# Performance work log

Hardware: AMD Instinct MI355X
Metric: run time of the kernel (lower is better)

The kernel has to match this reference:

```python
import jax, jax.numpy as jnp
import numpy as np

M, N = 4096, 4096


def _makhoul_perm(n):
    # Makhoul even/odd reordering: v[k] = x[2k] for k < ceil(n/2),
    # v[n-1-k] = x[2k+1] for the rest. This is the same input permutation
    # the dct2_fft2 kernel applies before its rfft2.
    idx = np.empty(n, dtype=np.int32)
    half = (n + 1) // 2
    idx[:half] = 2 * np.arange(half)
    idx[half:] = 2 * (n - 1 - np.arange(half, n)) + 1
    return jnp.asarray(idx)


def _dct2_1d_last(x):
    # Unnormalized DCT-II along the last axis via a same-length FFT plus
    # twiddle (expk) multiply:  C[k] = Re( exp(-i*pi*k/(2n)) * FFT(v)[k] )
    # which equals sum_m x[m] * cos(pi*k*(2m+1)/(2n)).
    n = x.shape[-1]
    v = jnp.take(x, _makhoul_perm(n), axis=-1)
    V = jnp.fft.fft(v, axis=-1)
    k = jnp.arange(n)
    expk = jnp.exp((-1j * np.pi / (2.0 * n)) * k)  # twiddle factors (expkM/expkN)
    return jnp.real(V * expk).astype(x.dtype)


def setup_inputs() -> dict:
    key = jax.random.key(0)
    x = jax.random.normal(key, (M, N), dtype=jnp.float32)
    return {"x": x}


def reference(x):
    # Separable 2D DCT-II: along axis -1 (uses expkN), then axis -2 (expkM).
    y = _dct2_1d_last(x)        # DCT over columns index (length N)
    y = _dct2_1d_last(y.T).T    # DCT over rows index (length M)
    return y
```

## Files before the change

kernel.cpp:

```cpp
#include <hip/hip_runtime.h>
#include <stdint.h>


#define NF 4096

__device__ __forceinline__ int physi(int e) { return e ^ ((e >> 4) & 15); }

__device__ __forceinline__ float2 cadd(float2 a, float2 b) {
    float2 r; r.x = a.x + b.x; r.y = a.y + b.y; return r;
}
__device__ __forceinline__ float2 csub(float2 a, float2 b) {
    float2 r; r.x = a.x - b.x; r.y = a.y - b.y; return r;
}
__device__ __forceinline__ float2 cmulc(float2 a, float2 b) {
    float2 r; r.x = a.x * b.x - a.y * b.y; r.y = a.x * b.y + a.y * b.x; return r;
}
__device__ __forceinline__ float2 rotm(float2 a) {
    float2 r; r.x = a.y; r.y = -a.x; return r;
}

__global__ __launch_bounds__(256) void setup_tables(float* __restrict__ tw,
                                                    float* __restrict__ ek) {
    int idx = blockIdx.x * 256 + threadIdx.x;
    if (idx < 4416) {
        int p, u; float denom;
        if (idx < 64)       { p = idx >> 3;         u = idx & 7;  denom = 64.0f; }
        else if (idx < 320) { int r = idx - 64;  p = r >> 4; u = r & 15; denom = 256.0f; }
        else                { int r = idx - 320; p = r >> 4; u = r & 15; denom = 4096.0f; }
        float phi = (float)(p * u) * (6.283185307179586f / denom);
        float s, c; __sincosf(phi, &s, &c);
        tw[2 * idx]     = c;
        tw[2 * idx + 1] = -s;
    } else if (idx < 8512) {
        int k = idx - 4416;
        float th = (float)k * (3.141592653589793f / 8192.0f);
        float s, c; __sincosf(th, &s, &c);
        ek[2 * k]     = c;
        ek[2 * k + 1] = s;
    }
}

#define RADIX8(Xv, E0, E1, E2, E3, O0, g1, g2, g3)                             \
    float2 t0 = cadd(Xv[0], Xv[4]), t1 = csub(Xv[0], Xv[4]);                   \
    float2 t2 = cadd(Xv[2], Xv[6]), t3 = csub(Xv[2], Xv[6]);                   \
    float2 E0 = cadd(t0, t2), E2 = csub(t0, t2);                               \
    float2 r3 = rotm(t3);                                                      \
    float2 E1 = cadd(t1, r3), E3 = csub(t1, r3);                               \
    float2 s0 = cadd(Xv[1], Xv[5]), s1 = csub(Xv[1], Xv[5]);                   \
    float2 s2 = cadd(Xv[3], Xv[7]), s3 = csub(Xv[3], Xv[7]);                   \
    float2 O0 = cadd(s0, s2), O2 = csub(s0, s2);                               \
    float2 r7 = rotm(s3);                                                      \
    float2 O1 = cadd(s1, r7), O3 = csub(s1, r7);                               \
    const float SQ = 0.7071067811865476f;                                      \
    float2 g1; g1.x = SQ * (O1.x + O1.y); g1.y = SQ * (O1.y - O1.x);           \
    float2 g2 = rotm(O2);                                                      \
    float2 g3; g3.x = SQ * (O3.y - O3.x); g3.y = -SQ * (O3.x + O3.y);

#define RADIX8_OUT(Xv, Ov)                                                     \
    {                                                                          \
        RADIX8(Xv, E0, E1, E2, E3, O0, g1, g2, g3)                             \
        Ov[0] = cadd(E0, O0); Ov[1] = cadd(E1, g1);                            \
        Ov[2] = cadd(E2, g2); Ov[3] = cadd(E3, g3);                            \
        Ov[4] = csub(E0, O0); Ov[5] = csub(E1, g1);                            \
        Ov[6] = csub(E2, g2); Ov[7] = csub(E3, g3);                            \
    }

__device__ __forceinline__ void dft16(float2* x) {
    float2 E[8], O[8];
    {
        float2 a[8];
        #pragma unroll
        for (int m = 0; m < 8; ++m) a[m] = x[2 * m];
        RADIX8_OUT(a, E)
    }
    {
        float2 a[8];
        #pragma unroll
        for (int m = 0; m < 8; ++m) a[m] = x[2 * m + 1];
        RADIX8_OUT(a, O)
    }
    const float2 W1 = { 0.9238795325112867f, -0.3826834323650898f};
    const float2 W2 = { 0.7071067811865476f, -0.7071067811865476f};
    const float2 W3 = { 0.3826834323650898f, -0.9238795325112867f};
    const float2 W5 = {-0.3826834323650898f, -0.9238795325112867f};
    const float2 W6 = {-0.7071067811865476f, -0.7071067811865476f};
    const float2 W7 = {-0.9238795325112867f, -0.3826834323650898f};
    float2 t;
    x[0] = cadd(E[0], O[0]);  x[8]  = csub(E[0], O[0]);
    t = cmulc(O[1], W1); x[1] = cadd(E[1], t); x[9]  = csub(E[1], t);
    t = cmulc(O[2], W2); x[2] = cadd(E[2], t); x[10] = csub(E[2], t);
    t = cmulc(O[3], W3); x[3] = cadd(E[3], t); x[11] = csub(E[3], t);
    t = rotm(O[4]);      x[4] = cadd(E[4], t); x[12] = csub(E[4], t);
    t = cmulc(O[5], W5); x[5] = cadd(E[5], t); x[13] = csub(E[5], t);
    t = cmulc(O[6], W6); x[6] = cadd(E[6], t); x[14] = csub(E[6], t);
    t = cmulc(O[7], W7); x[7] = cadd(E[7], t); x[15] = csub(E[7], t);
}

__global__ __launch_bounds__(256) void dct_rows(const float* __restrict__ In,
                                                float* __restrict__ Out,
                                                const float* __restrict__ tw,
                                                const float* __restrict__ ek) {
    __shared__ float2 buf[NF];
    const int j = threadIdx.x;
    const int b = blockIdx.x;
    const float* in0 = In + (size_t)(2 * b) * NF;
    const float* in1 = in0 + NF;
    float* out0 = Out + (size_t)b * NF;
    float* out1 = Out + (size_t)(4095 - b) * NF;

    const float4* i40 = (const float4*)in0;
    const float4* i41 = (const float4*)in1;
    #pragma unroll
    for (int c = 0; c < 4; ++c) {
        float4 a0 = i40[j + 256 * c];
        float4 a1 = i41[j + 256 * c];
        int nb = 2 * j + 512 * c;
        float2 z0; z0.x = a0.x; z0.y = a1.x;
        float2 z1; z1.x = a0.z; z1.y = a1.z;
        float2 z2; z2.x = a0.y; z2.y = a1.y;
        float2 z3; z3.x = a0.w; z3.y = a1.w;
        buf[physi(nb)]        = z0;
        buf[physi(nb + 1)]    = z1;
        buf[physi(4095 - nb)] = z2;
        buf[physi(4094 - nb)] = z3;
    }
    __syncthreads();

    float2 x[16];

    #pragma unroll
    for (int k = 0; k < 16; ++k)
        x[k] = buf[physi(j + 256 * k)];
    dft16(x);
    __syncthreads();
    #pragma unroll
    for (int i = 0; i < 16; ++i)
        buf[physi(16 * j + i)] = x[i];
    __syncthreads();

    {
        const int p = j & 15, q = j >> 4;
        #pragma unroll
        for (int k = 0; k < 16; ++k)
            x[k] = buf[physi(j + 256 * k)];
        const float2* twp = (const float2*)tw + 64 + p * 16;
        #pragma unroll
        for (int k = 1; k < 16; ++k)
            x[k] = cmulc(x[k], twp[k]);
        dft16(x);
        __syncthreads();
        int wb = p + 256 * q;
        #pragma unroll
        for (int i = 0; i < 16; ++i)
            buf[physi(wb + 16 * i)] = x[i];
        __syncthreads();
    }

    {
        #pragma unroll
        for (int k = 0; k < 16; ++k)
            x[k] = buf[physi(j + 256 * k)];
        const float2* twp = (const float2*)tw + 320 + j * 16;
        #pragma unroll
        for (int k = 1; k < 16; ++k)
            x[k] = cmulc(x[k], twp[k]);
        dft16(x);
        #pragma unroll
        for (int i = 0; i < 16; ++i)
            buf[physi(j + 256 * i)] = x[i];
    }
    __syncthreads();

    #pragma unroll
    for (int i = 0; i < 16; ++i) {
        int k = j + 256 * i;
        int m = (NF - k) & (NF - 1);
        float2 Zk = x[i];
        float2 Zm = buf[physi(m)];
        float2 E = ((const float2*)ek)[k];
        out0[k] = 0.5f * ((Zk.x + Zm.x) * E.x + (Zk.y - Zm.y) * E.y);
        out1[k] = 0.5f * ((Zk.y + Zm.y) * E.x - (Zk.x - Zm.x) * E.y);
    }
}

__global__ __launch_bounds__(256) void col_fft1(const float* __restrict__ V,
                                                float* __restrict__ S,
                                                const float* __restrict__ tw) {
    __shared__ float2 T[64][64];
    __shared__ float2 w64[64];
    const int ct = blockIdx.x, n1 = blockIdx.y;
    const int t = threadIdx.x;
    const int cp4 = t & 31, j = t >> 5;
    const float4* in4 = (const float4*)V + (size_t)ct * 32 + cp4;

    if (t < 64) {
        int m = (n1 * t) & 4095;
        float phi = (float)m * -1.5339807878856412e-3f;
        float s, c; __sincosf(phi, &s, &c);
        float2 w; w.x = c; w.y = s;
        w64[t] = w;
    }

    float2 xA[8], xB[8];
    #pragma unroll
    for (int k = 0; k < 8; ++k) {
        float4 v4 = in4[(size_t)(n1 + 64 * (j + 8 * k)) * 1024];
        xA[k].x = v4.x; xA[k].y = v4.y;
        xB[k].x = v4.z; xB[k].y = v4.w;
    }
    {
        float2 rA[8], rB[8];
        RADIX8_OUT(xA, rA)
        RADIX8_OUT(xB, rB)
        #pragma unroll
        for (int i = 0; i < 8; ++i) {
            float4 w; w.x = rA[i].x; w.y = rA[i].y; w.z = rB[i].x; w.w = rB[i].y;
            *(float4*)&T[8 * j + i][2 * cp4] = w;
        }
    }
    __syncthreads();

    float2 oA[8], oB[8];
    {
        #pragma unroll
        for (int k = 0; k < 8; ++k) {
            float4 v4 = *(const float4*)&T[j + 8 * k][2 * cp4];
            xA[k].x = v4.x; xA[k].y = v4.y;
            xB[k].x = v4.z; xB[k].y = v4.w;
        }
        const float2* twp = (const float2*)tw + j * 8;
        #pragma unroll
        for (int k = 1; k < 8; ++k) {
            xA[k] = cmulc(xA[k], twp[k]);
            xB[k] = cmulc(xB[k], twp[k]);
        }
        RADIX8_OUT(xA, oA)
        RADIX8_OUT(xB, oB)
    }

    float4* out4 = (float4*)S + (size_t)ct * 32 + cp4;
    #pragma unroll
    for (int i = 0; i < 8; ++i) {
        int k2 = j + 8 * i;
        float2 hA = cmulc(oA[i], w64[k2]);
        float2 hB = cmulc(oB[i], w64[k2]);
        float4 w; w.x = hA.x; w.y = hA.y; w.z = hB.x; w.w = hB.y;
        out4[(size_t)(64 * k2 + n1) * 1024] = w;
    }
}

__global__ __launch_bounds__(512) void col_fft2(const float* __restrict__ S,
                                                float* __restrict__ Out,
                                                const float* __restrict__ tw,
                                                const float* __restrict__ ek) {
    __shared__ float2 T[2][64][32];
    const int ct = blockIdx.x, bp = blockIdx.y;
    const int ga = bp, gb = (bp == 0) ? 32 : 64 - bp;
    const int t = threadIdx.x;
    const int cp = t & 31, j = (t >> 5) & 7, gi = t >> 8;
    const int g = gi ? gb : ga;
    const float2* inb = (const float2*)S + (size_t)ct * 32 + cp;

    float2 x[8];
    #pragma unroll
    for (int k = 0; k < 8; ++k)
        x[k] = inb[(size_t)(64 * g + j + 8 * k) * 2048];
    {
        float2 r[8];
        RADIX8_OUT(x, r)
        #pragma unroll
        for (int i = 0; i < 8; ++i)
            T[gi][8 * j + i][cp] = r[i];
    }
    __syncthreads();

    float2 o[8];
    {
        #pragma unroll
        for (int k = 0; k < 8; ++k)
            x[k] = T[gi][j + 8 * k][cp];
        const float2* twp = (const float2*)tw + j * 8;
        #pragma unroll
        for (int k = 1; k < 8; ++k)
            x[k] = cmulc(x[k], twp[k]);
        RADIX8_OUT(x, o)
        #pragma unroll
        for (int i = 0; i < 8; ++i)
            T[gi][j + 8 * i][cp] = o[i];
    }
    __syncthreads();

    float2* outb = (float2*)Out + (size_t)ct * 32 + cp;
    #pragma unroll
    for (int i = 0; i < 8; ++i) {
        int k = 64 * (j + 8 * i) + g;
        int m = (NF - k) & (NF - 1);
        int gp = m & 63, k1p = m >> 6;
        float2 Zk = o[i];
        float2 Zm = T[(gp == ga) ? 0 : 1][k1p][cp];
        float2 E = ((const float2*)ek)[k];
        float2 r;
        r.x = 0.5f * ((Zk.x + Zm.x) * E.x + (Zk.y - Zm.y) * E.y);
        r.y = 0.5f * ((Zk.y + Zm.y) * E.x - (Zk.x - Zm.x) * E.y);
        outb[(size_t)k * 2048] = r;
    }
}

extern "C" void kernel_launch(void* const* d_in, const int* in_sizes, int n_in,
                              void* d_out, int out_size, void* d_ws, size_t ws_size,
                              hipStream_t stream) {
    const float* x = (const float*)d_in[0];
    float* out = (float*)d_out;

    float* tw = (float*)d_ws;
    float* ek = tw + 8832;
    float* B1 = ek + 8192;
    if (ws_size < (size_t)68096 + (size_t)NF * NF * sizeof(float)) return;

    setup_tables<<<34, 256, 0, stream>>>(tw, ek);
    dct_rows<<<NF / 2, 256, 0, stream>>>(x, out, tw, ek);
    col_fft1<<<dim3(32, 64), 256, 0, stream>>>(out, B1, tw);
    col_fft2<<<dim3(64, 32), 512, 0, stream>>>(B1, out, tw, ek);
}
```

Baseline: 167.6 us.

## Process four tiles per block with register prefetch of the next tile's global loads

All three FFT kernels now loop over four tiles per block, and the grids shrink by four. The next tile's global data is loaded into registers while the current tile is written to shared memory, so load latency overlaps with the FFT work. __syncthreads is replaced by a custom barrier that waits only on LDS counters, leaving the outstanding global prefetch loads in flight across the barrier. The cost is fewer blocks (512 or fewer per kernel) and higher register pressure, which may lower occupancy and parallelism on a 256-CU device.

```diff
diff --git a/kernel.cpp b/kernel.cpp
--- a/kernel.cpp
+++ b/kernel.cpp
@@ -3,6 +3,13 @@
 
 
 #define NF 4096
+
+#define LBAR()                                                                 \
+    do {                                                                       \
+        asm volatile("s_waitcnt lgkmcnt(0)" ::: "memory");                     \
+        __builtin_amdgcn_s_barrier();                                          \
+        __builtin_amdgcn_sched_barrier(0);                                     \
+    } while (0)
 
 __device__ __forceinline__ int physi(int e) { return e ^ ((e >> 4) & 15); }
 
@@ -102,84 +109,97 @@
                                                 const float* __restrict__ ek) {
     __shared__ float2 buf[NF];
     const int j = threadIdx.x;
-    const int b = blockIdx.x;
-    const float* in0 = In + (size_t)(2 * b) * NF;
-    const float* in1 = in0 + NF;
-    float* out0 = Out + (size_t)b * NF;
-    float* out1 = Out + (size_t)(4095 - b) * NF;
-
-    const float4* i40 = (const float4*)in0;
-    const float4* i41 = (const float4*)in1;
-    #pragma unroll
-    for (int c = 0; c < 4; ++c) {
-        float4 a0 = i40[j + 256 * c];
-        float4 a1 = i41[j + 256 * c];
-        int nb = 2 * j + 512 * c;
-        float2 z0; z0.x = a0.x; z0.y = a1.x;
-        float2 z1; z1.x = a0.z; z1.y = a1.z;
-        float2 z2; z2.x = a0.y; z2.y = a1.y;
-        float2 z3; z3.x = a0.w; z3.y = a1.w;
-        buf[physi(nb)]        = z0;
-        buf[physi(nb + 1)]    = z1;
-        buf[physi(4095 - nb)] = z2;
-        buf[physi(4094 - nb)] = z3;
-    }
-    __syncthreads();
-
-    float2 x[16];
-
-    #pragma unroll
-    for (int k = 0; k < 16; ++k)
-        x[k] = buf[physi(j + 256 * k)];
-    dft16(x);
-    __syncthreads();
-    #pragma unroll
-    for (int i = 0; i < 16; ++i)
-        buf[physi(16 * j + i)] = x[i];
-    __syncthreads();
-
-    {
-        const int p = j & 15, q = j >> 4;
+    const int b0 = blockIdx.x * 4;
+
+    float4 ca[4], cb[4];
+    {
+        const float4* i40 = (const float4*)(In + (size_t)(2 * b0) * NF);
+        const float4* i41 = i40 + 1024;
+        #pragma unroll
+        for (int c = 0; c < 4; ++c) { ca[c] = i40[j + 256 * c]; cb[c] = i41[j + 256 * c]; }
+    }
+
+    for (int tt = 0; tt < 4; ++tt) {
+        const int b = b0 + tt;
+        float* out0 = Out + (size_t)b * NF;
+        float* out1 = Out + (size_t)(4095 - b) * NF;
+
+        #pragma unroll
+        for (int c = 0; c < 4; ++c) {
+            int nb = 2 * j + 512 * c;
+            float2 z0; z0.x = ca[c].x; z0.y = cb[c].x;
+            float2 z1; z1.x = ca[c].z; z1.y = cb[c].z;
+            float2 z2; z2.x = ca[c].y; z2.y = cb[c].y;
+            float2 z3; z3.x = ca[c].w; z3.y = cb[c].w;
+            buf[physi(nb)]        = z0;
+            buf[physi(nb + 1)]    = z1;
+            buf[physi(4095 - nb)] = z2;
+            buf[physi(4094 - nb)] = z3;
+        }
+        if (tt < 3) {
+            const float4* n40 = (const float4*)(In + (size_t)(2 * (b + 1)) * NF);
+            const float4* n41 = n40 + 1024;
+            #pragma unroll
+            for (int c = 0; c < 4; ++c) { ca[c] = n40[j + 256 * c]; cb[c] = n41[j + 256 * c]; }
+        }
+        LBAR();
+
+        float2 x[16];
+
         #pragma unroll
         for (int k = 0; k < 16; ++k)
             x[k] = buf[physi(j + 256 * k)];
-        const float2* twp = (const float2*)tw + 64 + p * 16;
-        #pragma unroll
-        for (int k = 1; k < 16; ++k)
-            x[k] = cmulc(x[k], twp[k]);
         dft16(x);
-        __syncthreads();
-        int wb = p + 256 * q;
+        LBAR();
         #pragma unroll
         for (int i = 0; i < 16; ++i)
-            buf[physi(wb + 16 * i)] = x[i];
-        __syncthreads();
-    }
-
-    {
-        #pragma unroll
-        for (int k = 0; k < 16; ++k)
-            x[k] = buf[physi(j + 256 * k)];
-        const float2* twp = (const float2*)tw + 320 + j * 16;
-        #pragma unroll
-        for (int k = 1; k < 16; ++k)
-            x[k] = cmulc(x[k], twp[k]);
-        dft16(x);
-        #pragma unroll
-        for (int i = 0; i < 16; ++i)
-            buf[physi(j + 256 * i)] = x[i];
-    }
-    __syncthreads();
-
-    #pragma unroll
-    for (int i = 0; i < 16; ++i) {
-        int k = j + 256 * i;
-        int m = (NF - k) & (NF - 1);
-        float2 Zk = x[i];
-        float2 Zm = buf[physi(m)];
-        float2 E = ((const float2*)ek)[k];
-        out0[k] = 0.5f * ((Zk.x + Zm.x) * E.x + (Zk.y - Zm.y) * E.y);
-        out1[k] = 0.5f * ((Zk.y + Zm.y) * E.x - (Zk.x - Zm.x) * E.y);
+            buf[physi(16 * j + i)] = x[i];
+        LBAR();
+
+        {
+            const int p = j & 15, q = j >> 4;
+            #pragma unroll
+            for (int k = 0; k < 16; ++k)
+                x[k] = buf[physi(j + 256 * k)];
+            const float2* twp = (const float2*)tw + 64 + p * 16;
+            #pragma unroll
+            for (int k = 1; k < 16; ++k)
+                x[k] = cmulc(x[k], twp[k]);
+            dft16(x);
+            LBAR();
+            int wb = p + 256 * q;
+            #pragma unroll
+            for (int i = 0; i < 16; ++i)
+                buf[physi(wb + 16 * i)] = x[i];
+            LBAR();
+        }
+
+        {
+            #pragma unroll
+            for (int k = 0; k < 16; ++k)
+                x[k] = buf[physi(j + 256 * k)];
+            const float2* twp = (const float2*)tw + 320 + j * 16;
+            #pragma unroll
+            for (int k = 1; k < 16; ++k)
+                x[k] = cmulc(x[k], twp[k]);
+            dft16(x);
+            #pragma unroll
+            for (int i = 0; i < 16; ++i)
+                buf[physi(j + 256 * i)] = x[i];
+        }
+        LBAR();
+
+        #pragma unroll
+        for (int i = 0; i < 16; ++i) {
+            int k = j + 256 * i;
+            int m = (NF - k) & (NF - 1);
+            float2 Zk = x[i];
+            float2 Zm = buf[physi(m)];
+            float2 E = ((const float2*)ek)[k];
+            out0[k] = 0.5f * ((Zk.x + Zm.x) * E.x + (Zk.y - Zm.y) * E.y);
+            out1[k] = 0.5f * ((Zk.y + Zm.y) * E.x - (Zk.x - Zm.x) * E.y);
+        }
+        LBAR();
     }
 }
 
@@ -188,10 +208,9 @@
                                                 const float* __restrict__ tw) {
     __shared__ float2 T[64][64];
     __shared__ float2 w64[64];
-    const int ct = blockIdx.x, n1 = blockIdx.y;
+    const int ct0 = blockIdx.x * 4, n1 = blockIdx.y;
     const int t = threadIdx.x;
     const int cp4 = t & 31, j = t >> 5;
-    const float4* in4 = (const float4*)V + (size_t)ct * 32 + cp4;
 
     if (t < 64) {
         int m = (n1 * t) & 4095;
@@ -201,51 +220,69 @@
         w64[t] = w;
     }
 
-    float2 xA[8], xB[8];
-    #pragma unroll
-    for (int k = 0; k < 8; ++k) {
-        float4 v4 = in4[(size_t)(n1 + 64 * (j + 8 * k)) * 1024];
-        xA[k].x = v4.x; xA[k].y = v4.y;
-        xB[k].x = v4.z; xB[k].y = v4.w;
-    }
-    {
-        float2 rA[8], rB[8];
-        RADIX8_OUT(xA, rA)
-        RADIX8_OUT(xB, rB)
-        #pragma unroll
-        for (int i = 0; i < 8; ++i) {
-            float4 w; w.x = rA[i].x; w.y = rA[i].y; w.z = rB[i].x; w.w = rB[i].y;
-            *(float4*)&T[8 * j + i][2 * cp4] = w;
-        }
-    }
-    __syncthreads();
-
-    float2 oA[8], oB[8];
-    {
-        #pragma unroll
-        for (int k = 0; k < 8; ++k) {
-            float4 v4 = *(const float4*)&T[j + 8 * k][2 * cp4];
-            xA[k].x = v4.x; xA[k].y = v4.y;
-            xB[k].x = v4.z; xB[k].y = v4.w;
-        }
-        const float2* twp = (const float2*)tw + j * 8;
-        #pragma unroll
-        for (int k = 1; k < 8; ++k) {
-            xA[k] = cmulc(xA[k], twp[k]);
-            xB[k] = cmulc(xB[k], twp[k]);
-        }
-        RADIX8_OUT(xA, oA)
-        RADIX8_OUT(xB, oB)
-    }
-
-    float4* out4 = (float4*)S + (size_t)ct * 32 + cp4;
-    #pragma unroll
-    for (int i = 0; i < 8; ++i) {
-        int k2 = j + 8 * i;
-        float2 hA = cmulc(oA[i], w64[k2]);
-        float2 hB = cmulc(oB[i], w64[k2]);
-        float4 w; w.x = hA.x; w.y = hA.y; w.z = hB.x; w.w = hB.y;
-        out4[(size_t)(64 * k2 + n1) * 1024] = w;
+    float4 pf[8];
+    {
+        const float4* in4 = (const float4*)V + (size_t)ct0 * 32 + cp4;
+        #pragma unroll
+        for (int k = 0; k < 8; ++k)
+            pf[k] = in4[(size_t)(n1 + 64 * (j + 8 * k)) * 1024];
+    }
+
+    for (int tt = 0; tt < 4; ++tt) {
+        const int ct = ct0 + tt;
+
+        {
+            float2 xA[8], xB[8];
+            #pragma unroll
+            for (int k = 0; k < 8; ++k) {
+                xA[k].x = pf[k].x; xA[k].y = pf[k].y;
+                xB[k].x = pf[k].z; xB[k].y = pf[k].w;
+            }
+            float2 rA[8], rB[8];
+            RADIX8_OUT(xA, rA)
+            RADIX8_OUT(xB, rB)
+            #pragma unroll
+            for (int i = 0; i < 8; ++i) {
+                float4 w; w.x = rA[i].x; w.y = rA[i].y; w.z = rB[i].x; w.w = rB[i].y;
+                *(float4*)&T[8 * j + i][2 * cp4] = w;
+            }
+        }
+        if (tt < 3) {
+            const float4* n4 = (const float4*)V + (size_t)(ct + 1) * 32 + cp4;
+            #pragma unroll
+            for (int k = 0; k < 8; ++k)
+                pf[k] = n4[(size_t)(n1 + 64 * (j + 8 * k)) * 1024];
+        }
+        LBAR();
+
+        {
+            float2 xA[8], xB[8], oA[8], oB[8];
+            #pragma unroll
+            for (int k = 0; k < 8; ++k) {
+                float4 v4 = *(const float4*)&T[j + 8 * k][2 * cp4];
+                xA[k].x = v4.x; xA[k].y = v4.y;
+                xB[k].x = v4.z; xB[k].y = v4.w;
+            }
+            const float2* twp = (const float2*)tw + j * 8;
+            #pragma unroll
+            for (int k = 1; k < 8; ++k) {
+                xA[k] = cmulc(xA[k], twp[k]);
+                xB[k] = cmulc(xB[k], twp[k]);
+            }
+            RADIX8_OUT(xA, oA)
+            RADIX8_OUT(xB, oB)
+
+            float4* out4 = (float4*)S + (size_t)ct * 32 + cp4;
+            #pragma unroll
+            for (int i = 0; i < 8; ++i) {
+                int k2 = j + 8 * i;
+                float2 hA = cmulc(oA[i], w64[k2]);
+                float2 hB = cmulc(oB[i], w64[k2]);
+                float4 w; w.x = hA.x; w.y = hA.y; w.z = hB.x; w.w = hB.y;
+                out4[(size_t)(64 * k2 + n1) * 1024] = w;
+            }
+        }
+        LBAR();
     }
 }
 
@@ -254,55 +291,72 @@
                                                 const float* __restrict__ tw,
                                                 const float* __restrict__ ek) {
     __shared__ float2 T[2][64][32];
-    const int ct = blockIdx.x, bp = blockIdx.y;
+    const int ct0 = blockIdx.x * 4, bp = blockIdx.y;
     const int ga = bp, gb = (bp == 0) ? 32 : 64 - bp;
     const int t = threadIdx.x;
     const int cp = t & 31, j = (t >> 5) & 7, gi = t >> 8;
     const int g = gi ? gb : ga;
-    const float2* inb = (const float2*)S + (size_t)ct * 32 + cp;
-
-    float2 x[8];
-    #pragma unroll
-    for (int k = 0; k < 8; ++k)
-        x[k] = inb[(size_t)(64 * g + j + 8 * k) * 2048];
-    {
-        float2 r[8];
-        RADIX8_OUT(x, r)
-        #pragma unroll
-        for (int i = 0; i < 8; ++i)
-            T[gi][8 * j + i][cp] = r[i];
-    }
-    __syncthreads();
-
-    float2 o[8];
-    {
+
+    float2 pf[8];
+    {
+        const float2* inb = (const float2*)S + (size_t)ct0 * 32 + cp;
         #pragma unroll
         for (int k = 0; k < 8; ++k)
-            x[k] = T[gi][j + 8 * k][cp];
-        const float2* twp = (const float2*)tw + j * 8;
-        #pragma unroll
-        for (int k = 1; k < 8; ++k)
-            x[k] = cmulc(x[k], twp[k]);
-        RADIX8_OUT(x, o)
-        #pragma unroll
-        for (int i = 0; i < 8; ++i)
-            T[gi][j + 8 * i][cp] = o[i];
-    }
-    __syncthreads();
-
-    float2* outb = (float2*)Out + (size_t)ct * 32 + cp;
-    #pragma unroll
-    for (int i = 0; i < 8; ++i) {
-        int k = 64 * (j + 8 * i) + g;
-        int m = (NF - k) & (NF - 1);
-        int gp = m & 63, k1p = m >> 6;
-        float2 Zk = o[i];
-        float2 Zm = T[(gp == ga) ? 0 : 1][k1p][cp];
-        float2 E = ((const float2*)ek)[k];
-        float2 r;
-        r.x = 0.5f * ((Zk.x + Zm.x) * E.x + (Zk.y - Zm.y) * E.y);
-        r.y = 0.5f * ((Zk.y + Zm.y) * E.x - (Zk.x - Zm.x) * E.y);
-        outb[(size_t)k * 2048] = r;
+            pf[k] = inb[(size_t)(64 * g + j + 8 * k) * 2048];
+    }
+
+    for (int tt = 0; tt < 4; ++tt) {
+        const int ct = ct0 + tt;
+
+        {
+            float2 r[8];
+            RADIX8_OUT(pf, r)
+            #pragma unroll
+            for (int i = 0; i < 8; ++i)
+                T[gi][8 * j + i][cp] = r[i];
+        }
+        if (tt < 3) {
+            const float2* nb = (const float2*)S + (size_t)(ct + 1) * 32 + cp;
+            #pragma unroll
+            for (int k = 0; k < 8; ++k)
+                pf[k] = nb[(size_t)(64 * g + j + 8 * k) * 2048];
+        }
+        LBAR();
+
+        float2 o[8];
+        {
+            float2 x[8];
+            #pragma unroll
+            for (int k = 0; k < 8; ++k)
+                x[k] = T[gi][j + 8 * k][cp];
+            const float2* twp = (const float2*)tw + j * 8;
+            #pragma unroll
+            for (int k = 1; k < 8; ++k)
+                x[k] = cmulc(x[k], twp[k]);
+            RADIX8_OUT(x, o)
+            #pragma unroll
+            for (int i = 0; i < 8; ++i)
+                T[gi][j + 8 * i][cp] = o[i];
+        }
+        LBAR();
+
+        {
+            float2* outb = (float2*)Out + (size_t)ct * 32 + cp;
+            #pragma unroll
+            for (int i = 0; i < 8; ++i) {
+                int k = 64 * (j + 8 * i) + g;
+                int m = (NF - k) & (NF - 1);
+                int gp = m & 63, k1p = m >> 6;
+                float2 Zk = o[i];
+                float2 Zm = T[(gp == ga) ? 0 : 1][k1p][cp];
+                float2 E = ((const float2*)ek)[k];
+                float2 r;
+                r.x = 0.5f * ((Zk.x + Zm.x) * E.x + (Zk.y - Zm.y) * E.y);
+                r.y = 0.5f * ((Zk.y + Zm.y) * E.x - (Zk.x - Zm.x) * E.y);
+                outb[(size_t)k * 2048] = r;
+            }
+        }
+        LBAR();
     }
 }
 
@@ -318,7 +372,7 @@
     if (ws_size < (size_t)68096 + (size_t)NF * NF * sizeof(float)) return;
 
     setup_tables<<<34, 256, 0, stream>>>(tw, ek);
-    dct_rows<<<NF / 2, 256, 0, stream>>>(x, out, tw, ek);
-    col_fft1<<<dim3(32, 64), 256, 0, stream>>>(out, B1, tw);
-    col_fft2<<<dim3(64, 32), 512, 0, stream>>>(B1, out, tw, ek);
-}
+    dct_rows<<<NF / 8, 256, 0, stream>>>(x, out, tw, ek);
+    col_fft1<<<dim3(8, 64), 256, 0, stream>>>(out, B1, tw);
+    col_fft2<<<dim3(16, 32), 512, 0, stream>>>(B1, out, tw, ek);
+}
```

Result: slower. 176.6 us (+5.4%).

## Fuse two-pass column FFT into single in-LDS 4096-point column DCT kernel

Applied to the files above, without the earlier changes.

Replaces the two column FFT kernels, which went through a global scratch buffer, with one kernel that loads four complex columns (a 4096x8 float strip) into 128 KB of dynamic LDS. It runs three radix-16 stages in shared memory with a swizzled index to avoid bank conflicts, then applies the DCT post-processing in place. This removes a full 64 MB round trip through global memory and one launch. In exchange it allows only one 1024-thread block per CU, leaves just 512 blocks, and adds more LDS barriers. Block ordering is interleaved across column tiles.

```diff
diff --git a/kernel.cpp b/kernel.cpp
--- a/kernel.cpp
+++ b/kernel.cpp
@@ -5,6 +5,10 @@
 #define NF 4096
 
 __device__ __forceinline__ int physi(int e) { return e ^ ((e >> 4) & 15); }
+
+__device__ __forceinline__ int cfi(int n, int c) {
+    return (n << 2) | (c ^ (((n >> 2) ^ (n >> 4)) & 3));
+}
 
 __device__ __forceinline__ float2 cadd(float2 a, float2 b) {
     float2 r; r.x = a.x + b.x; r.y = a.y + b.y; return r;
@@ -183,126 +187,87 @@
     }
 }
 
-__global__ __launch_bounds__(256) void col_fft1(const float* __restrict__ V,
-                                                float* __restrict__ S,
-                                                const float* __restrict__ tw) {
-    __shared__ float2 T[64][64];
-    __shared__ float2 w64[64];
-    const int ct = blockIdx.x, n1 = blockIdx.y;
-    const int t = threadIdx.x;
-    const int cp4 = t & 31, j = t >> 5;
-    const float4* in4 = (const float4*)V + (size_t)ct * 32 + cp4;
-
-    if (t < 64) {
-        int m = (n1 * t) & 4095;
-        float phi = (float)m * -1.5339807878856412e-3f;
-        float s, c; __sincosf(phi, &s, &c);
-        float2 w; w.x = c; w.y = s;
-        w64[t] = w;
-    }
-
-    float2 xA[8], xB[8];
-    #pragma unroll
-    for (int k = 0; k < 8; ++k) {
-        float4 v4 = in4[(size_t)(n1 + 64 * (j + 8 * k)) * 1024];
-        xA[k].x = v4.x; xA[k].y = v4.y;
-        xB[k].x = v4.z; xB[k].y = v4.w;
-    }
-    {
-        float2 rA[8], rB[8];
-        RADIX8_OUT(xA, rA)
-        RADIX8_OUT(xB, rB)
-        #pragma unroll
-        for (int i = 0; i < 8; ++i) {
-            float4 w; w.x = rA[i].x; w.y = rA[i].y; w.z = rB[i].x; w.w = rB[i].y;
-            *(float4*)&T[8 * j + i][2 * cp4] = w;
-        }
-    }
-    __syncthreads();
-
-    float2 oA[8], oB[8];
-    {
-        #pragma unroll
-        for (int k = 0; k < 8; ++k) {
-            float4 v4 = *(const float4*)&T[j + 8 * k][2 * cp4];
-            xA[k].x = v4.x; xA[k].y = v4.y;
-            xB[k].x = v4.z; xB[k].y = v4.w;
-        }
-        const float2* twp = (const float2*)tw + j * 8;
-        #pragma unroll
-        for (int k = 1; k < 8; ++k) {
-            xA[k] = cmulc(xA[k], twp[k]);
-            xB[k] = cmulc(xB[k], twp[k]);
-        }
-        RADIX8_OUT(xA, oA)
-        RADIX8_OUT(xB, oB)
-    }
-
-    float4* out4 = (float4*)S + (size_t)ct * 32 + cp4;
-    #pragma unroll
-    for (int i = 0; i < 8; ++i) {
-        int k2 = j + 8 * i;
-        float2 hA = cmulc(oA[i], w64[k2]);
-        float2 hB = cmulc(oB[i], w64[k2]);
-        float4 w; w.x = hA.x; w.y = hA.y; w.z = hB.x; w.w = hB.y;
-        out4[(size_t)(64 * k2 + n1) * 1024] = w;
-    }
-}
-
-__global__ __launch_bounds__(512) void col_fft2(const float* __restrict__ S,
-                                                float* __restrict__ Out,
+__global__ __launch_bounds__(1024) void col_dct(float* __restrict__ Out,
                                                 const float* __restrict__ tw,
                                                 const float* __restrict__ ek) {
-    __shared__ float2 T[2][64][32];
-    const int ct = blockIdx.x, bp = blockIdx.y;
-    const int ga = bp, gb = (bp == 0) ? 32 : 64 - bp;
+    extern __shared__ float2 buf[];
     const int t = threadIdx.x;
-    const int cp = t & 31, j = (t >> 5) & 7, gi = t >> 8;
-    const int g = gi ? gb : ga;
-    const float2* inb = (const float2*)S + (size_t)ct * 32 + cp;
-
-    float2 x[8];
-    #pragma unroll
-    for (int k = 0; k < 8; ++k)
-        x[k] = inb[(size_t)(64 * g + j + 8 * k) * 2048];
-    {
-        float2 r[8];
-        RADIX8_OUT(x, r)
-        #pragma unroll
-        for (int i = 0; i < 8; ++i)
-            T[gi][8 * j + i][cp] = r[i];
-    }
-    __syncthreads();
-
-    float2 o[8];
-    {
-        #pragma unroll
-        for (int k = 0; k < 8; ++k)
-            x[k] = T[gi][j + 8 * k][cp];
-        const float2* twp = (const float2*)tw + j * 8;
-        #pragma unroll
-        for (int k = 1; k < 8; ++k)
-            x[k] = cmulc(x[k], twp[k]);
-        RADIX8_OUT(x, o)
-        #pragma unroll
-        for (int i = 0; i < 8; ++i)
-            T[gi][j + 8 * i][cp] = o[i];
-    }
-    __syncthreads();
-
-    float2* outb = (float2*)Out + (size_t)ct * 32 + cp;
-    #pragma unroll
-    for (int i = 0; i < 8; ++i) {
-        int k = 64 * (j + 8 * i) + g;
+    const int bi = blockIdx.x;
+    const int ct = (bi & 7) * 64 + (bi >> 3);
+    const int c = t & 3;
+    const int j = t >> 2;
+    float* base = Out + 8 * (size_t)ct;
+
+    {
+        const int h = t & 1, r0 = t >> 1;
+        #pragma unroll
+        for (int k = 0; k < 8; ++k) {
+            int r = r0 + 512 * k;
+            float4 v = *(const float4*)&base[(size_t)r * NF + 4 * h];
+            float2 a; a.x = v.x; a.y = v.y;
+            float2 d; d.x = v.z; d.y = v.w;
+            buf[cfi(r, 2 * h)]     = a;
+            buf[cfi(r, 2 * h + 1)] = d;
+        }
+    }
+    __syncthreads();
+
+    float2 x[16];
+
+    #pragma unroll
+    for (int k = 0; k < 16; ++k)
+        x[k] = buf[cfi(j + 256 * k, c)];
+    dft16(x);
+    __syncthreads();
+    #pragma unroll
+    for (int i = 0; i < 16; ++i)
+        buf[cfi(16 * j + i, c)] = x[i];
+    __syncthreads();
+
+    {
+        const int p = j & 15, q = j >> 4;
+        #pragma unroll
+        for (int k = 0; k < 16; ++k)
+            x[k] = buf[cfi(j + 256 * k, c)];
+        const float2* twp = (const float2*)tw + 64 + p * 16;
+        #pragma unroll
+        for (int k = 1; k < 16; ++k)
+            x[k] = cmulc(x[k], twp[k]);
+        dft16(x);
+        __syncthreads();
+        int wb = p + 256 * q;
+        #pragma unroll
+        for (int i = 0; i < 16; ++i)
+            buf[cfi(wb + 16 * i, c)] = x[i];
+        __syncthreads();
+    }
+
+    {
+        #pragma unroll
+        for (int k = 0; k < 16; ++k)
+            x[k] = buf[cfi(j + 256 * k, c)];
+        const float2* twp = (const float2*)tw + 320 + j * 16;
+        #pragma unroll
+        for (int k = 1; k < 16; ++k)
+            x[k] = cmulc(x[k], twp[k]);
+        dft16(x);
+        #pragma unroll
+        for (int i = 0; i < 16; ++i)
+            buf[cfi(j + 256 * i, c)] = x[i];
+    }
+    __syncthreads();
+
+    #pragma unroll
+    for (int i = 0; i < 16; ++i) {
+        int k = j + 256 * i;
         int m = (NF - k) & (NF - 1);
-        int gp = m & 63, k1p = m >> 6;
-        float2 Zk = o[i];
-        float2 Zm = T[(gp == ga) ? 0 : 1][k1p][cp];
+        float2 Zk = x[i];
+        float2 Zm = buf[cfi(m, c)];
         float2 E = ((const float2*)ek)[k];
         float2 r;
         r.x = 0.5f * ((Zk.x + Zm.x) * E.x + (Zk.y - Zm.y) * E.y);
         r.y = 0.5f * ((Zk.y + Zm.y) * E.x - (Zk.x - Zm.x) * E.y);
-        outb[(size_t)k * 2048] = r;
+        *(float2*)&base[(size_t)k * NF + 2 * c] = r;
     }
 }
 
@@ -314,11 +279,17 @@
 
     float* tw = (float*)d_ws;
     float* ek = tw + 8832;
-    float* B1 = ek + 8192;
-    if (ws_size < (size_t)68096 + (size_t)NF * NF * sizeof(float)) return;
+    if (ws_size < (size_t)68096) return;
+
+    static bool attr_done = false;
+    if (!attr_done) {
+        (void)hipFuncSetAttribute((const void*)col_dct,
+                                  hipFuncAttributeMaxDynamicSharedMemorySize,
+                                  131072);
+        attr_done = true;
+    }
 
     setup_tables<<<34, 256, 0, stream>>>(tw, ek);
     dct_rows<<<NF / 2, 256, 0, stream>>>(x, out, tw, ek);
-    col_fft1<<<dim3(32, 64), 256, 0, stream>>>(out, B1, tw);
-    col_fft2<<<dim3(64, 32), 512, 0, stream>>>(B1, out, tw, ek);
-}
+    col_dct<<<512, 1024, 131072, stream>>>(out, tw, ek);
+}
```

Result: no change. 169.4 us (+1.1%).
